# Performance work log

Hardware: AMD Instinct MI355X
Metric: run time of the kernel (lower is better)

## Reference

```python
import jax, jax.numpy as jnp
import numpy as np

N = 8192          # nodes in each graph
NODE_DIM = 128
HID = 128
OUT = 128
TOPK = 8
B = 4096          # batch_node_num
CTX = 31          # context_node_num
HEADS = 8
SOURCE = 4096
DROP_COL = 5
EXIST = 64        # exist_col = first 64 feature columns


def setup_inputs() -> dict:
    key = jax.random.key(0)
    ks = jax.random.split(key, 24)
    g = lambda i, shape, s=1.0: jax.random.normal(ks[i], shape, dtype=jnp.float32) * s
    inp = {}
    # graph data (adjacency scaled ~ normalized adjacency so activations stay sane)
    inp['adj'] = g(0, (N, N), 1.0 / np.sqrt(N))
    inp['graph'] = g(1, (N, N), 1.0 / np.sqrt(N))
    inp['node_emb_gcn'] = g(2, (N, NODE_DIM))
    inp['trainfeature'] = g(3, (N, NODE_DIM))
    inp['target_emb'] = g(4, (B, OUT))
    inp['batch_simi_node_feature'] = g(5, (B, TOPK, NODE_DIM))
    # buffers that the torch loops fully overwrite
    inp['node_emb_rd'] = jnp.zeros((B, CTX + 1, HID), jnp.float32)
    inp['feature'] = jnp.zeros((B, CTX + 1, NODE_DIM), jnp.float32)
    # index tensors
    inp['batch_node_idx'] = jax.random.randint(ks[6], (B,), 0, N, dtype=jnp.int32)
    inp['node_rd'] = jax.random.randint(ks[7], (B, CTX + 1), 0, N - SOURCE, dtype=jnp.int32)
    # learned parameters
    s_nd = 1.0 / np.sqrt(NODE_DIM); s_h = 1.0 / np.sqrt(HID)
    inp['translate_W'] = g(8, (NODE_DIM, HID), s_nd)
    inp['translate_b'] = jnp.zeros((HID,), jnp.float32)
    inp['paraForCos'] = g(9, (TOPK, 1), np.sqrt(2.0))
    inp['gcn_W'] = g(10, (NODE_DIM, HID), s_nd)
    inp['gcn_b'] = jnp.zeros((HID,), jnp.float32)
    inp['gcnE_W'] = g(11, (NODE_DIM, HID), s_nd)
    inp['gcnE_b'] = jnp.zeros((HID,), jnp.float32)
    inp['Wq'] = g(12, (HID, HID), s_h)
    inp['Wk'] = g(13, (HID, HID), s_h)
    inp['Wv'] = g(14, (HID, HID), s_h)
    inp['lin_W'] = g(15, (HID * 3, OUT), 1.0 / np.sqrt(HID * 3))
    inp['lin_b'] = jnp.zeros((OUT,), jnp.float32)
    return inp


def reference(adj, target_emb, node_emb_gcn, node_emb_rd, batch_node_idx,
              batch_simi_node_feature, graph, trainfeature, node_rd, feature,
              translate_W, translate_b, paraForCos, gcn_W, gcn_b,
              gcnE_W, gcnE_b, Wq, Wk, Wv, lin_W, lin_b):
    # translate + per-row paraForCos scaling (vectorized torch loop), mean over top_k
    bs = batch_simi_node_feature @ translate_W + translate_b        # [B, K, HID]
    simi_feature = jnp.mean(bs * paraForCos[None, :, :], axis=1)    # [B, HID]

    # single-layer GCNs: relu(A @ X @ W + b)
    emb_gcn = jax.nn.relu(adj @ (node_emb_gcn @ gcn_W) + gcn_b)     # [N, HID]
    emb_gcnE = jax.nn.relu(graph @ (trainfeature @ gcnE_W) + gcnE_b)

    # fused gather replacing the nested python loops:
    # row 0 of each batch entry is offset by `source`
    offs = jnp.where(jnp.arange(CTX + 1) == 0, SOURCE, 0).astype(node_rd.dtype)
    idx = node_rd + offs[None, :]                                   # [B, C+1]
    ner = emb_gcnE[idx]                                             # [B, C+1, HID]
    feat = trainfeature[idx]                                        # [B, C+1, NODE_DIM]

    emb_g = emb_gcn[batch_node_idx]                                 # [B, HID]

    # multi-head attention: target node (row 0) attends over all C+1 rows,
    # with a cosine-similarity bias on the existing feature columns
    dh = HID // HEADS
    q = (ner[:, 0, :] @ Wq).reshape(-1, HEADS, dh)                  # [B, H, dh]
    k = (ner @ Wk).reshape(-1, CTX + 1, HEADS, dh)                  # [B, C+1, H, dh]
    v = (ner @ Wv).reshape(-1, CTX + 1, HEADS, dh)
    fe = feat[:, :, :EXIST]
    fn = fe / (jnp.linalg.norm(fe, axis=-1, keepdims=True) + 1e-8)
    cos = jnp.einsum('bd,bcd->bc', fn[:, 0], fn)                    # [B, C+1]
    scores = jnp.einsum('bhd,bchd->bhc', q, k) / np.sqrt(dh) + cos[:, None, :]
    attn = jax.nn.softmax(scores, axis=-1)
    emb_att = jax.nn.elu(jnp.einsum('bhc,bchd->bhd', attn, v).reshape(-1, HID))

    final_emb = jnp.concatenate([emb_g, emb_att, simi_feature], axis=1)  # [B, 3*HID]
    result = final_emb @ lin_W + lin_b                              # [B, OUT]
    loss_ac = jnp.mean((target_emb[:, DROP_COL] - result[:, DROP_COL]) ** 2)
    return result, loss_ac
```

## Files before the change

kernel.cpp:

```cpp
#include <hip/hip_runtime.h>
#include <hip/hip_bf16.h>

#define NN 8192
#define ND 128
#define BSZ 4096
#define CTX1 32
#define SRC 4096
#define TOPK 8
#define DROPC 5

#define BM 16
#define BKC 512
#define NMS (NN / BKC)

using f4 = __attribute__((ext_vector_type(4))) float;
using bfrag = __attribute__((ext_vector_type(8))) short;

__device__ __forceinline__ short f2bf(float x) {
  __hip_bfloat16 h = __float2bfloat16(x);
  return __builtin_bit_cast(short, h);
}
__device__ __forceinline__ float bf2f(short s) {
  unsigned u = ((unsigned)(unsigned short)s) << 16;
  return __builtin_bit_cast(float, u);
}

__global__ __launch_bounds__(256) void prep_kernel(
    const float* __restrict__ trainfeature, const float* __restrict__ bsnf,
    const float* __restrict__ para, const float* __restrict__ lin_W,
    const float* __restrict__ Wq, const float* __restrict__ Wk,
    const float* __restrict__ Wv,
    float* __restrict__ tfn, float* __restrict__ wsum,
    float* __restrict__ meanpara, short* __restrict__ linWp,
    short* __restrict__ qkvWp) {
  int blk = blockIdx.x;
  int t = threadIdx.x;
  if (blk < 2048) {
    int row = blk * 4 + (t >> 6);
    int j = t & 63;
    float x = trainfeature[(size_t)row * ND + j];
    float ss = x * x;
    #pragma unroll
    for (int o = 32; o > 0; o >>= 1) ss += __shfl_xor(ss, o);
    float nrm = sqrtf(ss) + 1e-8f;
    tfn[(size_t)row * 64 + j] = x / nrm;
  } else if (blk < 4096) {
    int b = (blk - 2048) * 2 + (t >> 7);
    int k = t & 127;
    float s = 0.f;
    #pragma unroll
    for (int tt = 0; tt < TOPK; ++tt)
      s += para[tt] * bsnf[((size_t)b * TOPK + tt) * ND + k];
    wsum[(size_t)b * ND + k] = s * (1.0f / TOPK);
  } else if (blk == 4096) {
    if (t == 0) {
      float s = 0.f;
      for (int tt = 0; tt < TOPK; ++tt) s += para[tt];
      *meanpara = s * (1.0f / TOPK);
    }
  } else if (blk < 4109) {
    int kt = blk - 4097;
    #pragma unroll
    for (int q = 0; q < 16; ++q) {
      int e = t * 16 + q;
      int nt = e >> 9, lane = (e >> 3) & 63, j = e & 7;
      float v = lin_W[(size_t)(kt * 32 + (lane >> 4) * 8 + j) * 128 + nt * 16 + (lane & 15)];
      linWp[(size_t)kt * 4096 + e] = f2bf(v);
    }
  } else {
    int id = blk - 4109;
    int m = id >> 2, kt = id & 3;
    const float* Wm = m == 0 ? Wq : (m == 1 ? Wk : Wv);
    #pragma unroll
    for (int q = 0; q < 16; ++q) {
      int e = t * 16 + q;
      int nf = e >> 9, lane = (e >> 3) & 63, j = e & 7;
      float v = Wm[(size_t)(kt * 32 + (lane >> 4) * 8 + j) * 128 + nf * 16 + (lane & 15)];
      qkvWp[(size_t)((kt * 24 + m * 8 + nf) << 9) + (e & 511)] = f2bf(v);
    }
  }
}

__device__ __forceinline__ void gemm128_body(
    const float* __restrict__ A, const float* __restrict__ W,
    const float* __restrict__ bias, const float* __restrict__ bscale_ptr,
    float* __restrict__ Cf, short* __restrict__ Xpack, int row0) {
  __shared__ float Ws[128][132];
  __shared__ float As[64][128];
  int t = threadIdx.x;
  for (int i = t; i < 128 * 32; i += 256) {
    int r = i >> 5, c = (i & 31) * 4;
    *(f4*)&Ws[r][c] = *(const f4*)&W[(size_t)r * 128 + c];
  }
  for (int i = t; i < 64 * 32; i += 256) {
    int r = i >> 5, c = (i & 31) * 4;
    *(f4*)&As[r][c] = *(const f4*)&A[(size_t)(row0 + r) * 128 + c];
  }
  __syncthreads();
  int tr = (t >> 5) * 8;
  int tc = (t & 31) * 4;
  float acc[8][4];
  #pragma unroll
  for (int i = 0; i < 8; i++)
    #pragma unroll
    for (int j = 0; j < 4; j++) acc[i][j] = 0.f;
  for (int k = 0; k < 128; k++) {
    f4 w = *(const f4*)&Ws[k][tc];
    #pragma unroll
    for (int i = 0; i < 8; i++) {
      float a = As[tr + i][k];
      acc[i][0] = fmaf(a, w[0], acc[i][0]);
      acc[i][1] = fmaf(a, w[1], acc[i][1]);
      acc[i][2] = fmaf(a, w[2], acc[i][2]);
      acc[i][3] = fmaf(a, w[3], acc[i][3]);
    }
  }
  if (bias) {
    float bsc = bscale_ptr ? *bscale_ptr : 1.0f;
    #pragma unroll
    for (int i = 0; i < 8; i++)
      #pragma unroll
      for (int j = 0; j < 4; j++) acc[i][j] += bias[tc + j] * bsc;
  }
  if (Cf) {
    #pragma unroll
    for (int i = 0; i < 8; i++) {
      int r = row0 + tr + i;
      #pragma unroll
      for (int j = 0; j < 4; j++) Cf[(size_t)r * 128 + tc + j] = acc[i][j];
    }
  }
  if (Xpack) {
    int kb = row0 + tr;
    int kt = kb >> 5;
    int lane_hi = (kb >> 3) & 3;
    #pragma unroll
    for (int j = 0; j < 4; j++) {
      int n = tc + j;
      int ln = (n & 15) | (lane_hi << 4);
      bfrag h;
      #pragma unroll
      for (int i = 0; i < 8; i++) h[i] = f2bf(acc[i][j]);
      *(bfrag*)&Xpack[((size_t)(kt * 8 + (n >> 4)) * 64 + ln) * 8] = h;
    }
  }
}

__global__ __launch_bounds__(256) void gemm128_kernel(
    const float* __restrict__ A, const float* __restrict__ W,
    const float* __restrict__ bias, const float* __restrict__ bscale_ptr,
    float* __restrict__ Cf, short* __restrict__ Xpack) {
  gemm128_body(A, W, bias, bscale_ptr, Cf, Xpack, blockIdx.x * 64);
}

__global__ __launch_bounds__(256) void proj2_kernel(
    const float* __restrict__ A0, const float* __restrict__ W0, short* __restrict__ T0,
    const float* __restrict__ A1, const float* __restrict__ W1, short* __restrict__ T1) {
  if (blockIdx.y == 0)
    gemm128_body(A0, W0, nullptr, nullptr, nullptr, T0, blockIdx.x * 64);
  else
    gemm128_body(A1, W1, nullptr, nullptr, nullptr, T1, blockIdx.x * 64);
}

__global__ __launch_bounds__(256, 4) void big_gemm_kernel(
    const float* __restrict__ adj, const float* __restrict__ graphm,
    const short* __restrict__ XgP, const short* __restrict__ XEP,
    const int* __restrict__ bni,
    const float* __restrict__ gcnE_b, const float* __restrict__ gcn_b,
    const short* __restrict__ qkvWp,
    float* __restrict__ emb_gb, short* __restrict__ Qa_bf,
    short* __restrict__ Ka_bf, short* __restrict__ Va_bf) {
  const int bx0 = blockIdx.x;
  const int bx = (bx0 & 7) * 96 + (bx0 >> 3);
  const bool isG = bx >= 512;
  const int t = threadIdx.x;
  const int lane = t & 63;
  const int w = t >> 6;

  const float* __restrict__ Am = isG ? adj : graphm;
  const short* __restrict__ Xp = isG ? XgP : XEP;
  const int m0 = (isG ? bx - 512 : bx) * BM;

  const int sr = t >> 4;
  const int ss = t & 15;
  int grow = m0 + sr;
  if (isG) grow = bni[grow];
  const float* gsrc = Am + (size_t)grow * NN + ss * 32;

  __shared__ short Abuf[2][BM * BKC];

  const int fr = lane & 15;
  const int kq = lane >> 4;
  const short* Xb = Xp + (size_t)lane * 8;

  f4 acc0 = {0.f, 0.f, 0.f, 0.f}, acc1 = {0.f, 0.f, 0.f, 0.f};
  f4 st[8];
  #pragma unroll
  for (int i = 0; i < 8; i++) st[i] = *(const f4*)(gsrc + i * 4);

  for (int ms = 0; ms < NMS; ++ms) {
    const int cur = ms & 1;
    {
      short* rb = &Abuf[cur][sr * BKC];
      #pragma unroll
      for (int j = 0; j < 4; ++j) {
        bfrag h;
        #pragma unroll
        for (int e = 0; e < 8; ++e) h[e] = f2bf(st[j * 2 + (e >> 2)][e & 3]);
        int u_sw = (ss * 4 + j) ^ (sr & 7);
        *(bfrag*)&rb[u_sw * 8] = h;
      }
    }
    __syncthreads();
    if (ms + 1 < NMS) {
      const float* g2 = gsrc + (size_t)(ms + 1) * BKC;
      #pragma unroll
      for (int i = 0; i < 8; i++) st[i] = *(const f4*)(g2 + i * 4);
    }
    #pragma unroll
    for (int ks = 0; ks < 16; ++ks) {
      int u_sw = (ks * 4 + kq) ^ (fr & 7);
      bfrag a = *(const bfrag*)&Abuf[cur][fr * BKC + u_sw * 8];
      const short* xq = Xb + (size_t)(ms * 16 + ks) * 4096;
      bfrag b0 = *(const bfrag*)(xq + (2 * w) * 512);
      bfrag b1 = *(const bfrag*)(xq + (2 * w + 1) * 512);
      acc0 = __builtin_amdgcn_mfma_f32_16x16x32_bf16(a, b0, acc0, 0, 0, 0);
      acc1 = __builtin_amdgcn_mfma_f32_16x16x32_bf16(a, b1, acc1, 0, 0, 0);
    }
  }

  const int n0 = 2 * w * 16 + fr;
  if (isG) {
    const int orow = (bx - 512) * BM + kq * 4;
    #pragma unroll
    for (int r = 0; r < 4; ++r) {
      float v0 = fmaxf(acc0[r] + gcn_b[n0], 0.f);
      float v1 = fmaxf(acc1[r] + gcn_b[n0 + 16], 0.f);
      emb_gb[(size_t)(orow + r) * 128 + n0] = v0;
      emb_gb[(size_t)(orow + r) * 128 + n0 + 16] = v1;
    }
  } else {
    short* Et = &Abuf[0][0];
    #pragma unroll
    for (int r = 0; r < 4; ++r) {
      int rl = kq * 4 + r;
      Et[rl * 136 + n0] = f2bf(fmaxf(acc0[r] + gcnE_b[n0], 0.f));
      Et[rl * 136 + n0 + 16] = f2bf(fmaxf(acc1[r] + gcnE_b[n0 + 16], 0.f));
    }
    __syncthreads();
    bfrag af[4];
    #pragma unroll
    for (int kt = 0; kt < 4; ++kt)
      af[kt] = *(const bfrag*)&Et[fr * 136 + kt * 32 + kq * 8];
    f4 qacc[6];
    #pragma unroll
    for (int i = 0; i < 6; ++i) qacc[i] = (f4){0.f, 0.f, 0.f, 0.f};
    #pragma unroll
    for (int kt = 0; kt < 4; ++kt) {
      #pragma unroll
      for (int i = 0; i < 6; ++i) {
        int nfg = w * 6 + i;
        bfrag bb = *(const bfrag*)&qkvWp[((size_t)(kt * 24 + nfg) << 9) + lane * 8];
        qacc[i] = __builtin_amdgcn_mfma_f32_16x16x32_bf16(af[kt], bb, qacc[i], 0, 0, 0);
      }
    }
    #pragma unroll
    for (int i = 0; i < 6; ++i) {
      int nfg = w * 6 + i;
      int m = nfg >> 3, nf = nfg & 7;
      short* dst = m == 0 ? Qa_bf : (m == 1 ? Ka_bf : Va_bf);
      int col = nf * 16 + fr;
      #pragma unroll
      for (int r = 0; r < 4; ++r)
        dst[(size_t)(m0 + kq * 4 + r) * 128 + col] = f2bf(qacc[i][r]);
    }
  }
}

__global__ __launch_bounds__(128) void attn_kernel(
    const int* __restrict__ node_rd,
    const short* __restrict__ Qa_bf, const short* __restrict__ Ka_bf,
    const short* __restrict__ Va_bf, const float* __restrict__ tfn,
    const float* __restrict__ emb_gb, const float* __restrict__ simi,
    short* __restrict__ femb_bf) {
  int b = blockIdx.x;
  int t = threadIdx.x;
  __shared__ int idx[CTX1];
  __shared__ float tf0[64];
  __shared__ float qv[128];
  __shared__ float cosv[CTX1];
  __shared__ float sc[8][CTX1];

  if (t < CTX1) idx[t] = node_rd[(size_t)b * CTX1 + t] + (t == 0 ? SRC : 0);
  __syncthreads();
  int i0 = idx[0];
  if (t < 64) tf0[t] = tfn[(size_t)i0 * 64 + t];
  qv[t] = bf2f(Qa_bf[(size_t)i0 * 128 + t]);
  __syncthreads();

  {
    int c = t >> 2, q = t & 3;
    const float* tfc = tfn + (size_t)idx[c] * 64;
    float s = 0.f;
    #pragma unroll
    for (int j = 0; j < 16; j++) s += tf0[q + j * 4] * tfc[q + j * 4];
    s += __shfl_xor(s, 1);
    s += __shfl_xor(s, 2);
    if (q == 0) cosv[c] = s;
  }
  __syncthreads();

  for (int p = t; p < 256; p += 128) {
    int h = p >> 5, c = p & 31;
    const short* kp = Ka_bf + (size_t)idx[c] * 128 + h * 16;
    bfrag k0 = *(const bfrag*)(kp);
    bfrag k1 = *(const bfrag*)(kp + 8);
    float s = 0.f;
    #pragma unroll
    for (int j = 0; j < 8; j++) s += qv[h * 16 + j] * bf2f(k0[j]);
    #pragma unroll
    for (int j = 0; j < 8; j++) s += qv[h * 16 + 8 + j] * bf2f(k1[j]);
    sc[h][c] = s * 0.25f + cosv[c];
  }
  __syncthreads();

  {
    int h = t >> 4, l = t & 15;
    float s0 = sc[h][l], s1 = sc[h][l + 16];
    float m = fmaxf(s0, s1);
    #pragma unroll
    for (int o = 1; o < 16; o <<= 1) m = fmaxf(m, __shfl_xor(m, o));
    float e0 = expf(s0 - m), e1 = expf(s1 - m);
    float sum = e0 + e1;
    #pragma unroll
    for (int o = 1; o < 16; o <<= 1) sum += __shfl_xor(sum, o);
    float inv = 1.0f / sum;
    sc[h][l] = e0 * inv;
    sc[h][l + 16] = e1 * inv;
  }
  __syncthreads();

  {
    int h = t >> 4, d = t & 15;
    float o = 0.f;
    #pragma unroll 4
    for (int c = 0; c < CTX1; c++)
      o += sc[h][c] * bf2f(Va_bf[(size_t)idx[c] * 128 + h * 16 + d]);
    float e = (o > 0.f) ? o : expm1f(o);
    femb_bf[(size_t)b * 384 + 128 + t] = f2bf(e);
  }
  femb_bf[(size_t)b * 384 + t] = f2bf(emb_gb[(size_t)b * 128 + t]);
  femb_bf[(size_t)b * 384 + 256 + t] = f2bf(simi[(size_t)b * 128 + t]);
}

__global__ __launch_bounds__(64) void final_kernel(
    const short* __restrict__ femb_bf, const short* __restrict__ linWp,
    const float* __restrict__ lin_b, float* __restrict__ outr) {
  const int m0 = blockIdx.x * 16;
  const int lane = threadIdx.x;
  const int fr = lane & 15;
  const int kq = lane >> 4;
  f4 acc[8];
  #pragma unroll
  for (int i = 0; i < 8; i++) acc[i] = (f4){0.f, 0.f, 0.f, 0.f};
  #pragma unroll
  for (int kt = 0; kt < 12; ++kt) {
    bfrag a = *(const bfrag*)&femb_bf[(size_t)(m0 + fr) * 384 + kt * 32 + kq * 8];
    #pragma unroll
    for (int nt = 0; nt < 8; ++nt) {
      bfrag bb = *(const bfrag*)&linWp[(size_t)(kt * 8 + nt) * 512 + lane * 8];
      acc[nt] = __builtin_amdgcn_mfma_f32_16x16x32_bf16(a, bb, acc[nt], 0, 0, 0);
    }
  }
  #pragma unroll
  for (int nt = 0; nt < 8; ++nt) {
    int n = nt * 16 + fr;
    float bv = lin_b[n];
    #pragma unroll
    for (int r = 0; r < 4; ++r)
      outr[(size_t)(m0 + kq * 4 + r) * 128 + n] = acc[nt][r] + bv;
  }
}

__global__ __launch_bounds__(1024) void loss_kernel(
    const float* __restrict__ target, const float* __restrict__ result,
    float* __restrict__ out_loss) {
  int t = threadIdx.x;
  float s = 0.f;
  for (int b = t; b < BSZ; b += 1024) {
    float d = target[(size_t)b * 128 + DROPC] - result[(size_t)b * 128 + DROPC];
    s += d * d;
  }
  #pragma unroll
  for (int o = 32; o > 0; o >>= 1) s += __shfl_xor(s, o);
  __shared__ float red[16];
  if ((t & 63) == 0) red[t >> 6] = s;
  __syncthreads();
  if (t == 0) {
    float tot = 0.f;
    #pragma unroll
    for (int i = 0; i < 16; ++i) tot += red[i];
    out_loss[0] = tot * (1.0f / BSZ);
  }
}

extern "C" void kernel_launch(void* const* d_in, const int* in_sizes, int n_in,
                              void* d_out, int out_size, void* d_ws, size_t ws_size,
                              hipStream_t stream) {
  const float* adj = (const float*)d_in[0];
  const float* graphm = (const float*)d_in[1];
  const float* node_emb_gcn = (const float*)d_in[2];
  const float* trainfeature = (const float*)d_in[3];
  const float* target_emb = (const float*)d_in[4];
  const float* bsnf = (const float*)d_in[5];
  const int* batch_node_idx = (const int*)d_in[8];
  const int* node_rd = (const int*)d_in[9];
  const float* translate_W = (const float*)d_in[10];
  const float* translate_b = (const float*)d_in[11];
  const float* paraForCos = (const float*)d_in[12];
  const float* gcn_W = (const float*)d_in[13];
  const float* gcn_b = (const float*)d_in[14];
  const float* gcnE_W = (const float*)d_in[15];
  const float* gcnE_b = (const float*)d_in[16];
  const float* Wq = (const float*)d_in[17];
  const float* Wk = (const float*)d_in[18];
  const float* Wv = (const float*)d_in[19];
  const float* lin_W = (const float*)d_in[20];
  const float* lin_b = (const float*)d_in[21];

  char* ws = (char*)d_ws;
  size_t off = 0;
  auto alloc = [&](size_t bytes) {
    void* p = ws + off;
    off += (bytes + 255) & ~(size_t)255;
    return p;
  };
  short* XgP = (short*)alloc((size_t)128 * NN * 2);
  short* XEP = (short*)alloc((size_t)128 * NN * 2);
  float* tfn = (float*)alloc((size_t)NN * 64 * 4);
  float* wsum = (float*)alloc((size_t)BSZ * 128 * 4);
  float* simi = (float*)alloc((size_t)BSZ * 128 * 4);
  short* Qa_bf = (short*)alloc((size_t)NN * 128 * 2);
  short* Ka_bf = (short*)alloc((size_t)NN * 128 * 2);
  short* Va_bf = (short*)alloc((size_t)NN * 128 * 2);
  float* emb_gb = (float*)alloc((size_t)BSZ * 128 * 4);
  float* meanpara = (float*)alloc(256);
  short* femb_bf = (short*)alloc((size_t)BSZ * 384 * 2);
  short* linWp = (short*)alloc((size_t)12 * 4096 * 2);
  short* qkvWp = (short*)alloc((size_t)4 * 24 * 512 * 2);

  float* out_res = (float*)d_out;
  float* out_loss = out_res + (size_t)BSZ * 128;

  prep_kernel<<<4121, 256, 0, stream>>>(trainfeature, bsnf, paraForCos, lin_W,
                                        Wq, Wk, Wv, tfn, wsum, meanpara, linWp, qkvWp);
  proj2_kernel<<<dim3(NN / 64, 2), 256, 0, stream>>>(node_emb_gcn, gcn_W, XgP,
                                                     trainfeature, gcnE_W, XEP);
  big_gemm_kernel<<<768, 256, 0, stream>>>(adj, graphm, XgP, XEP, batch_node_idx,
                                           gcnE_b, gcn_b, qkvWp, emb_gb,
                                           Qa_bf, Ka_bf, Va_bf);
  gemm128_kernel<<<BSZ / 64, 256, 0, stream>>>(wsum, translate_W, translate_b, meanpara,
                                               simi, nullptr);
  attn_kernel<<<BSZ, 128, 0, stream>>>(node_rd, Qa_bf, Ka_bf, Va_bf, tfn, emb_gb,
                                       simi, femb_bf);
  final_kernel<<<BSZ / 16, 64, 0, stream>>>(femb_bf, linWp, lin_b, out_res);
  loss_kernel<<<1, 1024, 0, stream>>>(target_emb, out_res, out_loss);
}
```

Measured before the change: 219.2 us.

## Fold translate GEMM into big_gemm via MFMA blocks and halve K-chunk size

The separate fp32 translate GEMM kernel is removed. Its work runs as 64 extra blocks appended to big_gemm_kernel, using bf16 MFMA with translate_W pre-packed in prep_kernel. This saves one launch and lets the small GEMM overlap the large adjacency GEMM. The adjacency staging chunk is also halved (BKC 512→256) with launch bounds raised to 8 blocks per CU, cutting LDS and register use to allow more occupancy, at the cost of more sync iterations and bf16 precision for the simi path.

```diff
diff --git a/kernel.cpp b/kernel.cpp
--- a/kernel.cpp
+++ b/kernel.cpp
@@ -10,7 +10,7 @@
 #define DROPC 5
 
 #define BM 16
-#define BKC 512
+#define BKC 256
 #define NMS (NN / BKC)
 
 using f4 = __attribute__((ext_vector_type(4))) float;
@@ -29,10 +29,10 @@
     const float* __restrict__ trainfeature, const float* __restrict__ bsnf,
     const float* __restrict__ para, const float* __restrict__ lin_W,
     const float* __restrict__ Wq, const float* __restrict__ Wk,
-    const float* __restrict__ Wv,
+    const float* __restrict__ Wv, const float* __restrict__ translate_W,
     float* __restrict__ tfn, float* __restrict__ wsum,
     float* __restrict__ meanpara, short* __restrict__ linWp,
-    short* __restrict__ qkvWp) {
+    short* __restrict__ qkvWp, short* __restrict__ twP) {
   int blk = blockIdx.x;
   int t = threadIdx.x;
   if (blk < 2048) {
@@ -67,7 +67,7 @@
       float v = lin_W[(size_t)(kt * 32 + (lane >> 4) * 8 + j) * 128 + nt * 16 + (lane & 15)];
       linWp[(size_t)kt * 4096 + e] = f2bf(v);
     }
-  } else {
+  } else if (blk < 4121) {
     int id = blk - 4109;
     int m = id >> 2, kt = id & 3;
     const float* Wm = m == 0 ? Wq : (m == 1 ? Wk : Wv);
@@ -78,12 +78,20 @@
       float v = Wm[(size_t)(kt * 32 + (lane >> 4) * 8 + j) * 128 + nf * 16 + (lane & 15)];
       qkvWp[(size_t)((kt * 24 + m * 8 + nf) << 9) + (e & 511)] = f2bf(v);
     }
+  } else {
+    int kt = blk - 4121;
+    #pragma unroll
+    for (int q = 0; q < 16; ++q) {
+      int e = t * 16 + q;
+      int nf = e >> 9, lane = (e >> 3) & 63, j = e & 7;
+      float v = translate_W[(size_t)(kt * 32 + (lane >> 4) * 8 + j) * 128 + nf * 16 + (lane & 15)];
+      twP[(size_t)((kt * 8 + nf) << 9) + (e & 511)] = f2bf(v);
+    }
   }
 }
 
 __device__ __forceinline__ void gemm128_body(
     const float* __restrict__ A, const float* __restrict__ W,
-    const float* __restrict__ bias, const float* __restrict__ bscale_ptr,
     float* __restrict__ Cf, short* __restrict__ Xpack, int row0) {
   __shared__ float Ws[128][132];
   __shared__ float As[64][128];
@@ -115,13 +123,6 @@
       acc[i][3] = fmaf(a, w[3], acc[i][3]);
     }
   }
-  if (bias) {
-    float bsc = bscale_ptr ? *bscale_ptr : 1.0f;
-    #pragma unroll
-    for (int i = 0; i < 8; i++)
-      #pragma unroll
-      for (int j = 0; j < 4; j++) acc[i][j] += bias[tc + j] * bsc;
-  }
   if (Cf) {
     #pragma unroll
     for (int i = 0; i < 8; i++) {
@@ -146,37 +147,64 @@
   }
 }
 
-__global__ __launch_bounds__(256) void gemm128_kernel(
-    const float* __restrict__ A, const float* __restrict__ W,
-    const float* __restrict__ bias, const float* __restrict__ bscale_ptr,
-    float* __restrict__ Cf, short* __restrict__ Xpack) {
-  gemm128_body(A, W, bias, bscale_ptr, Cf, Xpack, blockIdx.x * 64);
-}
-
 __global__ __launch_bounds__(256) void proj2_kernel(
     const float* __restrict__ A0, const float* __restrict__ W0, short* __restrict__ T0,
     const float* __restrict__ A1, const float* __restrict__ W1, short* __restrict__ T1) {
   if (blockIdx.y == 0)
-    gemm128_body(A0, W0, nullptr, nullptr, nullptr, T0, blockIdx.x * 64);
+    gemm128_body(A0, W0, nullptr, T0, blockIdx.x * 64);
   else
-    gemm128_body(A1, W1, nullptr, nullptr, nullptr, T1, blockIdx.x * 64);
-}
-
-__global__ __launch_bounds__(256, 4) void big_gemm_kernel(
+    gemm128_body(A1, W1, nullptr, T1, blockIdx.x * 64);
+}
+
+__global__ __launch_bounds__(256, 8) void big_gemm_kernel(
     const float* __restrict__ adj, const float* __restrict__ graphm,
     const short* __restrict__ XgP, const short* __restrict__ XEP,
     const int* __restrict__ bni,
     const float* __restrict__ gcnE_b, const float* __restrict__ gcn_b,
     const short* __restrict__ qkvWp,
+    const float* __restrict__ wsum, const short* __restrict__ twP,
+    const float* __restrict__ translate_b, const float* __restrict__ meanpara,
     float* __restrict__ emb_gb, short* __restrict__ Qa_bf,
-    short* __restrict__ Ka_bf, short* __restrict__ Va_bf) {
+    short* __restrict__ Ka_bf, short* __restrict__ Va_bf,
+    float* __restrict__ simi) {
   const int bx0 = blockIdx.x;
-  const int bx = (bx0 & 7) * 96 + (bx0 >> 3);
-  const bool isG = bx >= 512;
   const int t = threadIdx.x;
   const int lane = t & 63;
   const int w = t >> 6;
-
+  const int fr = lane & 15;
+  const int kq = lane >> 4;
+
+  if (bx0 >= 768) {
+    const int m0 = (bx0 - 768) * 64 + w * 16;
+    const float mp = *meanpara;
+    f4 acc[8];
+    #pragma unroll
+    for (int i = 0; i < 8; i++) acc[i] = (f4){0.f, 0.f, 0.f, 0.f};
+    #pragma unroll
+    for (int kt = 0; kt < 4; ++kt) {
+      const float* ap = wsum + (size_t)(m0 + fr) * 128 + kt * 32 + kq * 8;
+      bfrag a;
+      #pragma unroll
+      for (int j = 0; j < 8; ++j) a[j] = f2bf(ap[j]);
+      #pragma unroll
+      for (int nt = 0; nt < 8; ++nt) {
+        bfrag bb = *(const bfrag*)&twP[(size_t)((kt * 8 + nt) << 9) + lane * 8];
+        acc[nt] = __builtin_amdgcn_mfma_f32_16x16x32_bf16(a, bb, acc[nt], 0, 0, 0);
+      }
+    }
+    #pragma unroll
+    for (int nt = 0; nt < 8; ++nt) {
+      int n = nt * 16 + fr;
+      float bv = translate_b[n] * mp;
+      #pragma unroll
+      for (int r = 0; r < 4; ++r)
+        simi[(size_t)(m0 + kq * 4 + r) * 128 + n] = acc[nt][r] + bv;
+    }
+    return;
+  }
+
+  const int bx = (bx0 & 7) * 96 + (bx0 >> 3);
+  const bool isG = bx >= 512;
   const float* __restrict__ Am = isG ? adj : graphm;
   const short* __restrict__ Xp = isG ? XgP : XEP;
   const int m0 = (isG ? bx - 512 : bx) * BM;
@@ -185,29 +213,27 @@
   const int ss = t & 15;
   int grow = m0 + sr;
   if (isG) grow = bni[grow];
-  const float* gsrc = Am + (size_t)grow * NN + ss * 32;
+  const float* gsrc = Am + (size_t)grow * NN + ss * 16;
 
   __shared__ short Abuf[2][BM * BKC];
 
-  const int fr = lane & 15;
-  const int kq = lane >> 4;
   const short* Xb = Xp + (size_t)lane * 8;
 
   f4 acc0 = {0.f, 0.f, 0.f, 0.f}, acc1 = {0.f, 0.f, 0.f, 0.f};
-  f4 st[8];
-  #pragma unroll
-  for (int i = 0; i < 8; i++) st[i] = *(const f4*)(gsrc + i * 4);
+  f4 st[4];
+  #pragma unroll
+  for (int i = 0; i < 4; i++) st[i] = *(const f4*)(gsrc + i * 4);
 
   for (int ms = 0; ms < NMS; ++ms) {
     const int cur = ms & 1;
     {
       short* rb = &Abuf[cur][sr * BKC];
       #pragma unroll
-      for (int j = 0; j < 4; ++j) {
+      for (int j = 0; j < 2; ++j) {
         bfrag h;
         #pragma unroll
         for (int e = 0; e < 8; ++e) h[e] = f2bf(st[j * 2 + (e >> 2)][e & 3]);
-        int u_sw = (ss * 4 + j) ^ (sr & 7);
+        int u_sw = (ss * 2 + j) ^ (sr & 7);
         *(bfrag*)&rb[u_sw * 8] = h;
       }
     }
@@ -215,13 +241,13 @@
     if (ms + 1 < NMS) {
       const float* g2 = gsrc + (size_t)(ms + 1) * BKC;
       #pragma unroll
-      for (int i = 0; i < 8; i++) st[i] = *(const f4*)(g2 + i * 4);
-    }
-    #pragma unroll
-    for (int ks = 0; ks < 16; ++ks) {
+      for (int i = 0; i < 4; i++) st[i] = *(const f4*)(g2 + i * 4);
+    }
+    #pragma unroll
+    for (int ks = 0; ks < 8; ++ks) {
       int u_sw = (ks * 4 + kq) ^ (fr & 7);
       bfrag a = *(const bfrag*)&Abuf[cur][fr * BKC + u_sw * 8];
-      const short* xq = Xb + (size_t)(ms * 16 + ks) * 4096;
+      const short* xq = Xb + (size_t)(ms * 8 + ks) * 4096;
       bfrag b0 = *(const bfrag*)(xq + (2 * w) * 512);
       bfrag b1 = *(const bfrag*)(xq + (2 * w + 1) * 512);
       acc0 = __builtin_amdgcn_mfma_f32_16x16x32_bf16(a, b0, acc0, 0, 0, 0);
@@ -448,19 +474,20 @@
   short* femb_bf = (short*)alloc((size_t)BSZ * 384 * 2);
   short* linWp = (short*)alloc((size_t)12 * 4096 * 2);
   short* qkvWp = (short*)alloc((size_t)4 * 24 * 512 * 2);
+  short* twP = (short*)alloc((size_t)4 * 8 * 512 * 2);
 
   float* out_res = (float*)d_out;
   float* out_loss = out_res + (size_t)BSZ * 128;
 
-  prep_kernel<<<4121, 256, 0, stream>>>(trainfeature, bsnf, paraForCos, lin_W,
-                                        Wq, Wk, Wv, tfn, wsum, meanpara, linWp, qkvWp);
+  prep_kernel<<<4125, 256, 0, stream>>>(trainfeature, bsnf, paraForCos, lin_W,
+                                        Wq, Wk, Wv, translate_W,
+                                        tfn, wsum, meanpara, linWp, qkvWp, twP);
   proj2_kernel<<<dim3(NN / 64, 2), 256, 0, stream>>>(node_emb_gcn, gcn_W, XgP,
                                                      trainfeature, gcnE_W, XEP);
-  big_gemm_kernel<<<768, 256, 0, stream>>>(adj, graphm, XgP, XEP, batch_node_idx,
-                                           gcnE_b, gcn_b, qkvWp, emb_gb,
-                                           Qa_bf, Ka_bf, Va_bf);
-  gemm128_kernel<<<BSZ / 64, 256, 0, stream>>>(wsum, translate_W, translate_b, meanpara,
-                                               simi, nullptr);
+  big_gemm_kernel<<<832, 256, 0, stream>>>(adj, graphm, XgP, XEP, batch_node_idx,
+                                           gcnE_b, gcn_b, qkvWp, wsum, twP,
+                                           translate_b, meanpara, emb_gb,
+                                           Qa_bf, Ka_bf, Va_bf, simi);
   attn_kernel<<<BSZ, 128, 0, stream>>>(node_rd, Qa_bf, Ka_bf, Va_bf, tfn, emb_gb,
                                        simi, femb_bf);
   final_kernel<<<BSZ / 16, 64, 0, stream>>>(femb_bf, linWp, lin_b, out_res);
```

New measurement: 194.3 us, median of 2. -11.4%, faster.
